# Optimization experiments

Measured on AMD Instinct MI355X. Metric: run time of the kernel, lower is better.

Reference implementation:

```python
import jax, jax.numpy as jnp
import numpy as np

# Vehicle / drivetrain constants (match init_kwargs and hard-coded source constants)
LF, LR = 1.5, 1.4
CM1, CM2 = 550.0, 650.0
MASS, IZ = 1265.0, 2000.0
DT = 0.01
C_DRIVE = 3.45 * 0.919 / (0.34 * 1265.0)  # gear-ratio constant from source
GRAV = 9.8


def _mlp(a, w1, b1, w2, b2):
    # 1 -> 12 -> 1 MLP applied per-row. a: [B]; w1,b1,w2: [12]; b2: scalar
    h = jax.nn.relu(a[:, None] * w1[None, :] + b1[None, :])  # [B, 12]
    return h @ w2 + b2  # [B]


def setup_inputs() -> dict:
    key = jax.random.key(0)
    ks = jax.random.split(key, 7)
    B = 4_194_304
    x = jax.random.normal(ks[0], (B, 8), dtype=jnp.float32)
    # First-layer init as in source: weight filled with 1.0, bias = arange(-0.6, 0.6, 0.1)
    b1 = (-0.6 + 0.1 * jnp.arange(12)).astype(jnp.float32)
    bound = float(1.0 / np.sqrt(12.0))  # torch default init bound for Linear(12, 1)
    return {
        "x": x,
        "fy_w1": jnp.ones((12,), jnp.float32),
        "fy_b1": b1,
        "fy_w2": jax.random.uniform(ks[1], (12,), jnp.float32, -bound, bound),
        "fy_b2": jax.random.uniform(ks[2], (), jnp.float32, -bound, bound),
        "ry_w1": jnp.ones((12,), jnp.float32),
        "ry_b1": b1,
        "ry_w2": jax.random.uniform(ks[3], (12,), jnp.float32, -bound, bound),
        "ry_b2": jax.random.uniform(ks[4], (), jnp.float32, -bound, bound),
        "rx_w": jax.random.uniform(ks[5], (), jnp.float32, -1.0, 1.0),
        "rx_b": jax.random.uniform(ks[6], (), jnp.float32, -1.0, 1.0),
    }


def reference(x, fy_w1, fy_b1, fy_w2, fy_b2, ry_w1, ry_b1, ry_w2, ry_b2, rx_w, rx_b):
    pwm = x[:, 0]
    theta = x[:, 2]
    pitch = x[:, 7]
    out = jnp.zeros_like(x[:, 3:6])  # [B, 3] accumulated (dvx, dvy, dw)

    def fy(a):
        return _mlp(a, fy_w1, fy_b1, fy_w2, fy_b2)

    def ry(a):
        return _mlp(a, ry_w1, ry_b1, ry_w2, ry_b2)

    st, ct = jnp.sin(theta), jnp.cos(theta)
    sp = jnp.sin(pitch)
    a_pred = jnp.where(pwm > 0.0, CM1, CM2) * pwm * C_DRIVE

    for _ in range(2):  # fixed 2-step integration loop, as in source
        vx = x[:, 3] + out[:, 0]
        vy = x[:, 4] + out[:, 1]
        w = x[:, 5] + out[:, 2]
        alpha_f = theta - jnp.arctan2(w * LF + vy, vx)
        alpha_r = jnp.arctan2(w * LR - vy, vx)
        # Fy(a)*(a>0) - Fy(-a)*(a<=0): exactly one branch survives per element
        Ffy = jnp.where(alpha_f > 0.0, fy(alpha_f), -fy(-alpha_f))
        Fry = jnp.where(alpha_r > 0.0, ry(alpha_r), -ry(-alpha_r))
        Frx = a_pred + rx_w * vx * vx + rx_b  # Rx(vx^2) + drivetrain accel
        vx_dot = Frx - Ffy * st + vy * w - GRAV * sp
        vy_dot = Fry + Ffy * ct - vx * w
        w_dot = MASS * (Ffy * LF * ct - Fry * LR) / IZ
        out = out + DT * jnp.stack([vx_dot, vy_dot, w_dot], axis=1)
    return out
```

## Files before the change

kernel.cpp:

```cpp
#include <hip/hip_runtime.h>
#include <math.h>

#define DEV_INLINE __device__ __forceinline__

DEV_INLINE float fast_atan2f(float y, float x) {
    const float kPI  = 3.14159265358979323846f;
    const float kPI2 = 1.57079632679489661923f;
    float ax = fabsf(x), ay = fabsf(y);
    float mx = fmaxf(ax, ay);
    float mn = fminf(ax, ay);
    float a  = mn * __builtin_amdgcn_rcpf(mx);
    float s  = a * a;
    float p  = -0.01172120f;
    p = fmaf(p, s,  0.05265332f);
    p = fmaf(p, s, -0.11643287f);
    p = fmaf(p, s,  0.19354346f);
    p = fmaf(p, s, -0.33262347f);
    p = fmaf(p, s,  0.99997726f);
    float r = a * p;
    r = (ay > ax)   ? (kPI2 - r) : r;
    r = (x < 0.0f)  ? (kPI  - r) : r;
    return copysignf(r, y);
}

DEV_INLINE float mlp12(float a, const float* __restrict__ w1,
                       const float* __restrict__ b1,
                       const float* __restrict__ w2, float b2) {
    float acc = b2;
#pragma unroll
    for (int j = 0; j < 12; ++j) {
        float h = fmaxf(fmaf(a, w1[j], b1[j]), 0.0f);
        acc = fmaf(h, w2[j], acc);
    }
    return acc;
}

DEV_INLINE void compute_row(float pwm, float theta, float vx0, float vy0,
                            float w0, float pitch,
                            const float* fw1, const float* fb1, const float* fw2, float fb2,
                            const float* rw1, const float* rb1, const float* rw2, float rb2,
                            float rxw, float rxb,
                            float& o0, float& o1, float& o2) {
    const float kLF     = 1.5f;
    const float kLR     = 1.4f;
    const float kCM1    = 550.0f;
    const float kCM2    = 650.0f;
    const float kDT     = 0.01f;
    const float kGRAV   = 9.8f;
    const float kCDRIVE = (float)(3.45 * 0.919 / (0.34 * 1265.0));
    const float kWF     = (float)(1265.0 * 1.5 / 2000.0);
    const float kWR     = (float)(1265.0 * 1.4 / 2000.0);

    const float st = __sinf(theta);
    const float ct = __cosf(theta);
    const float sp = __sinf(pitch);
    const float a_pred = (pwm > 0.0f ? kCM1 : kCM2) * pwm * kCDRIVE;

    o0 = 0.0f; o1 = 0.0f; o2 = 0.0f;
#pragma unroll
    for (int it = 0; it < 2; ++it) {
        const float vx = vx0 + o0;
        const float vy = vy0 + o1;
        const float w  = w0  + o2;

        const float af = theta - fast_atan2f(fmaf(w, kLF, vy), vx);
        const float ar = fast_atan2f(fmaf(w, kLR, -vy), vx);

        const float sf  = af > 0.0f ? 1.0f : -1.0f;
        const float Ffy = sf * mlp12(sf * af, fw1, fb1, fw2, fb2);
        const float sr  = ar > 0.0f ? 1.0f : -1.0f;
        const float Fry = sr * mlp12(sr * ar, rw1, rb1, rw2, rb2);

        const float Frx = fmaf(rxw * vx, vx, a_pred + rxb);

        const float vx_dot = Frx - Ffy * st + vy * w - kGRAV * sp;
        const float vy_dot = Fry + Ffy * ct - vx * w;
        const float w_dot  = kWF * Ffy * ct - kWR * Fry;

        o0 = fmaf(kDT, vx_dot, o0);
        o1 = fmaf(kDT, vy_dot, o1);
        o2 = fmaf(kDT, w_dot,  o2);
    }
}

__global__ __launch_bounds__(256) void dyn_kernel(
    const float4* __restrict__ x4,
    const float* __restrict__ fy_w1, const float* __restrict__ fy_b1,
    const float* __restrict__ fy_w2, const float* __restrict__ fy_b2,
    const float* __restrict__ ry_w1, const float* __restrict__ ry_b1,
    const float* __restrict__ ry_w2, const float* __restrict__ ry_b2,
    const float* __restrict__ rx_w, const float* __restrict__ rx_b,
    float* __restrict__ out, int nrows) {
    __shared__ float sOut[1536];

    float fw1[12], fb1[12], fw2[12];
    float rw1[12], rb1[12], rw2[12];
#pragma unroll
    for (int j = 0; j < 12; ++j) {
        fw1[j] = fy_w1[j]; fb1[j] = fy_b1[j]; fw2[j] = fy_w2[j];
        rw1[j] = ry_w1[j]; rb1[j] = ry_b1[j]; rw2[j] = ry_w2[j];
    }
    const float fb2 = fy_b2[0];
    const float rb2 = ry_b2[0];
    const float rxw = rx_w[0];
    const float rxb = rx_b[0];

    const int tid = threadIdx.x;
    const long long rowBase = (long long)blockIdx.x * 512;
    const long long r0 = rowBase + tid;
    const long long r1 = rowBase + 256 + tid;

    float4 lo0 = make_float4(0.f, 0.f, 1.f, 0.f), hi0 = lo0;
    float4 lo1 = lo0, hi1 = lo0;
    if (r0 < nrows) { lo0 = x4[2 * r0]; hi0 = x4[2 * r0 + 1]; }
    if (r1 < nrows) { lo1 = x4[2 * r1]; hi1 = x4[2 * r1 + 1]; }

    float a0, a1, a2, b0, b1v, b2v;
    compute_row(lo0.x, lo0.z, lo0.w, hi0.x, hi0.y, hi0.w,
                fw1, fb1, fw2, fb2, rw1, rb1, rw2, rb2, rxw, rxb, a0, a1, a2);
    compute_row(lo1.x, lo1.z, lo1.w, hi1.x, hi1.y, hi1.w,
                fw1, fb1, fw2, fb2, rw1, rb1, rw2, rb2, rxw, rxb, b0, b1v, b2v);

    sOut[tid * 3 + 0] = a0;
    sOut[tid * 3 + 1] = a1;
    sOut[tid * 3 + 2] = a2;
    sOut[(256 + tid) * 3 + 0] = b0;
    sOut[(256 + tid) * 3 + 1] = b1v;
    sOut[(256 + tid) * 3 + 2] = b2v;
    __syncthreads();

    const long long gbase = rowBase * 3;
    const long long gmax  = (long long)nrows * 3;
#pragma unroll
    for (int j = 0; j < 6; ++j) {
        const long long gi = gbase + j * 256 + tid;
        if (gi < gmax) __builtin_nontemporal_store(sOut[j * 256 + tid], &out[gi]);
    }
}

extern "C" void kernel_launch(void* const* d_in, const int* in_sizes, int n_in,
                              void* d_out, int out_size, void* d_ws, size_t ws_size,
                              hipStream_t stream) {
    const float4* x4   = (const float4*)d_in[0];
    const float* fy_w1 = (const float*)d_in[1];
    const float* fy_b1 = (const float*)d_in[2];
    const float* fy_w2 = (const float*)d_in[3];
    const float* fy_b2 = (const float*)d_in[4];
    const float* ry_w1 = (const float*)d_in[5];
    const float* ry_b1 = (const float*)d_in[6];
    const float* ry_w2 = (const float*)d_in[7];
    const float* ry_b2 = (const float*)d_in[8];
    const float* rx_w  = (const float*)d_in[9];
    const float* rx_b  = (const float*)d_in[10];

    const int nrows = in_sizes[0] / 8;
    const int rows_per_block = 512;
    const int blocks = (nrows + rows_per_block - 1) / rows_per_block;

    dyn_kernel<<<blocks, 256, 0, stream>>>(
        x4, fy_w1, fy_b1, fy_w2, fy_b2, ry_w1, ry_b1, ry_w2, ry_b2, rx_w, rx_b,
        (float*)d_out, nrows);
}
```

Baseline: 224.5 us.

## Use persistent grid-stride loop with prefetch and shuffle-based output transpose

Replaces the one-shot 512-rows-per-block launch with a fixed 2048-block grid that loops over rows and prefetches the next row's inputs with nontemporal loads while computing the current one. The LDS staging and __syncthreads are replaced by wave-level shuffles that rearrange the three outputs into coalesced stores. The atan2 polynomial is switched to Estrin form and the MLP accumulation is split into four independent chains to shorten dependency latency. The aim is to overlap memory with compute and cut per-block overhead, at the cost of more shuffle instructions and fewer, longer-running blocks.

```diff
diff --git a/kernel.cpp b/kernel.cpp
--- a/kernel.cpp
+++ b/kernel.cpp
@@ -2,6 +2,8 @@
 #include <math.h>
 
 #define DEV_INLINE __device__ __forceinline__
+
+typedef float v4f __attribute__((ext_vector_type(4)));
 
 DEV_INLINE float fast_atan2f(float y, float x) {
     const float kPI  = 3.14159265358979323846f;
@@ -11,13 +13,13 @@
     float mn = fminf(ax, ay);
     float a  = mn * __builtin_amdgcn_rcpf(mx);
     float s  = a * a;
-    float p  = -0.01172120f;
-    p = fmaf(p, s,  0.05265332f);
-    p = fmaf(p, s, -0.11643287f);
-    p = fmaf(p, s,  0.19354346f);
-    p = fmaf(p, s, -0.33262347f);
-    p = fmaf(p, s,  0.99997726f);
-    float r = a * p;
+    float t0 = fmaf(s, -0.01172120f, 0.05265332f);
+    float t1 = fmaf(s, -0.11643287f, 0.19354346f);
+    float t2 = fmaf(s, -0.33262347f, 0.99997726f);
+    float s2 = s * s;
+    float u  = fmaf(t0, s2, t1);
+    float p  = fmaf(u, s2, t2);
+    float r  = a * p;
     r = (ay > ax)   ? (kPI2 - r) : r;
     r = (x < 0.0f)  ? (kPI  - r) : r;
     return copysignf(r, y);
@@ -26,13 +28,19 @@
 DEV_INLINE float mlp12(float a, const float* __restrict__ w1,
                        const float* __restrict__ b1,
                        const float* __restrict__ w2, float b2) {
-    float acc = b2;
+    float acc0 = b2, acc1 = 0.0f, acc2 = 0.0f, acc3 = 0.0f;
 #pragma unroll
-    for (int j = 0; j < 12; ++j) {
-        float h = fmaxf(fmaf(a, w1[j], b1[j]), 0.0f);
-        acc = fmaf(h, w2[j], acc);
+    for (int j = 0; j < 12; j += 4) {
+        float h0 = fmaxf(fmaf(a, w1[j + 0], b1[j + 0]), 0.0f);
+        float h1 = fmaxf(fmaf(a, w1[j + 1], b1[j + 1]), 0.0f);
+        float h2 = fmaxf(fmaf(a, w1[j + 2], b1[j + 2]), 0.0f);
+        float h3 = fmaxf(fmaf(a, w1[j + 3], b1[j + 3]), 0.0f);
+        acc0 = fmaf(h0, w2[j + 0], acc0);
+        acc1 = fmaf(h1, w2[j + 1], acc1);
+        acc2 = fmaf(h2, w2[j + 2], acc2);
+        acc3 = fmaf(h3, w2[j + 3], acc3);
     }
-    return acc;
+    return (acc0 + acc1) + (acc2 + acc3);
 }
 
 DEV_INLINE void compute_row(float pwm, float theta, float vx0, float vy0,
@@ -84,15 +92,13 @@
 }
 
 __global__ __launch_bounds__(256) void dyn_kernel(
-    const float4* __restrict__ x4,
+    const v4f* __restrict__ x4,
     const float* __restrict__ fy_w1, const float* __restrict__ fy_b1,
     const float* __restrict__ fy_w2, const float* __restrict__ fy_b2,
     const float* __restrict__ ry_w1, const float* __restrict__ ry_b1,
     const float* __restrict__ ry_w2, const float* __restrict__ ry_b2,
     const float* __restrict__ rx_w, const float* __restrict__ rx_b,
-    float* __restrict__ out, int nrows) {
-    __shared__ float sOut[1536];
-
+    float* __restrict__ out, int nrows, int nbatch) {
     float fw1[12], fb1[12], fw2[12];
     float rw1[12], rb1[12], rw2[12];
 #pragma unroll
@@ -105,43 +111,58 @@
     const float rxw = rx_w[0];
     const float rxb = rx_b[0];
 
-    const int tid = threadIdx.x;
-    const long long rowBase = (long long)blockIdx.x * 512;
-    const long long r0 = rowBase + tid;
-    const long long r1 = rowBase + 256 + tid;
+    const int tid  = threadIdx.x;
+    const int wave = tid >> 6;
+    const int lane = tid & 63;
 
-    float4 lo0 = make_float4(0.f, 0.f, 1.f, 0.f), hi0 = lo0;
-    float4 lo1 = lo0, hi1 = lo0;
-    if (r0 < nrows) { lo0 = x4[2 * r0]; hi0 = x4[2 * r0 + 1]; }
-    if (r1 < nrows) { lo1 = x4[2 * r1]; hi1 = x4[2 * r1 + 1]; }
+    const long long stride = (long long)gridDim.x * 256;
+    const long long gmax   = (long long)nrows * 3;
+    long long row = (long long)blockIdx.x * 256 + tid;
 
-    float a0, a1, a2, b0, b1v, b2v;
-    compute_row(lo0.x, lo0.z, lo0.w, hi0.x, hi0.y, hi0.w,
-                fw1, fb1, fw2, fb2, rw1, rb1, rw2, rb2, rxw, rxb, a0, a1, a2);
-    compute_row(lo1.x, lo1.z, lo1.w, hi1.x, hi1.y, hi1.w,
-                fw1, fb1, fw2, fb2, rw1, rb1, rw2, rb2, rxw, rxb, b0, b1v, b2v);
+    v4f lo = {0.f, 0.f, 0.f, 1.f};
+    v4f hi = {0.f, 0.f, 0.f, 0.f};
+    if (row < nrows) {
+        lo = __builtin_nontemporal_load(&x4[2 * row]);
+        hi = __builtin_nontemporal_load(&x4[2 * row + 1]);
+    }
 
-    sOut[tid * 3 + 0] = a0;
-    sOut[tid * 3 + 1] = a1;
-    sOut[tid * 3 + 2] = a2;
-    sOut[(256 + tid) * 3 + 0] = b0;
-    sOut[(256 + tid) * 3 + 1] = b1v;
-    sOut[(256 + tid) * 3 + 2] = b2v;
-    __syncthreads();
+    for (int k = 0; k < nbatch; ++k) {
+        const long long rown = row + stride;
+        v4f lon = {0.f, 0.f, 0.f, 1.f};
+        v4f hin = {0.f, 0.f, 0.f, 0.f};
+        if (k + 1 < nbatch && rown < nrows) {
+            lon = __builtin_nontemporal_load(&x4[2 * rown]);
+            hin = __builtin_nontemporal_load(&x4[2 * rown + 1]);
+        }
 
-    const long long gbase = rowBase * 3;
-    const long long gmax  = (long long)nrows * 3;
+        float o0, o1, o2;
+        compute_row(lo.x, lo.z, lo.w, hi.x, hi.y, hi.w,
+                    fw1, fb1, fw2, fb2, rw1, rb1, rw2, rb2, rxw, rxb,
+                    o0, o1, o2);
+
+        const long long gbase =
+            (k * stride + (long long)blockIdx.x * 256 + wave * 64) * 3;
 #pragma unroll
-    for (int j = 0; j < 6; ++j) {
-        const long long gi = gbase + j * 256 + tid;
-        if (gi < gmax) __builtin_nontemporal_store(sOut[j * 256 + tid], &out[gi]);
+        for (int j = 0; j < 3; ++j) {
+            const int p = j * 64 + lane;
+            const int r = p / 3;
+            const int c = p - r * 3;
+            const float v0 = __shfl(o0, r, 64);
+            const float v1 = __shfl(o1, r, 64);
+            const float v2 = __shfl(o2, r, 64);
+            const float val = (c == 0) ? v0 : ((c == 1) ? v1 : v2);
+            const long long gi = gbase + p;
+            if (gi < gmax) __builtin_nontemporal_store(val, &out[gi]);
+        }
+
+        row = rown; lo = lon; hi = hin;
     }
 }
 
 extern "C" void kernel_launch(void* const* d_in, const int* in_sizes, int n_in,
                               void* d_out, int out_size, void* d_ws, size_t ws_size,
                               hipStream_t stream) {
-    const float4* x4   = (const float4*)d_in[0];
+    const v4f* x4      = (const v4f*)d_in[0];
     const float* fy_w1 = (const float*)d_in[1];
     const float* fy_b1 = (const float*)d_in[2];
     const float* fy_w2 = (const float*)d_in[3];
@@ -154,10 +175,13 @@
     const float* rx_b  = (const float*)d_in[10];
 
     const int nrows = in_sizes[0] / 8;
-    const int rows_per_block = 512;
-    const int blocks = (nrows + rows_per_block - 1) / rows_per_block;
+    int blocks = 2048;
+    const int max_blocks = (nrows + 255) / 256;
+    if (blocks > max_blocks) blocks = max_blocks;
+    const long long stride = (long long)blocks * 256;
+    const int nbatch = (int)((nrows + stride - 1) / stride);
 
     dyn_kernel<<<blocks, 256, 0, stream>>>(
         x4, fy_w1, fy_b1, fy_w2, fy_b2, ry_w1, ry_b1, ry_w2, ry_b2, rx_w, rx_b,
-        (float*)d_out, nrows);
+        (float*)d_out, nrows, nbatch);
 }
```

Measured after the change: 227.8 us. About the same (+1.5%).
